# Kernel tuning notes

Hardware: AMD Instinct MI355X
Metric: run time of the kernel (lower is better)

Reference implementation:

```python
import jax, jax.numpy as jnp
import numpy as np

N = 50000
E = 800000
IN_CH = 128
HID = 32
HEADS = 8
OUT_CH = 64
NEG_SLOPE = 0.2  # PyG GATConv default


def setup_inputs() -> dict:
    key = jax.random.key(0)
    ks = jax.random.split(key, 12)
    x = jax.random.normal(ks[0], (N, IN_CH), dtype=jnp.float32)
    edge_index = jax.random.randint(ks[1], (2, E), 0, N, dtype=jnp.int64)
    s = 0.1
    return {
        "x": x,
        "edge_index": edge_index,
        "W1": jax.random.normal(ks[2], (IN_CH, HEADS * HID), dtype=jnp.float32) * s,
        "att_src1": jax.random.normal(ks[3], (HEADS, HID), dtype=jnp.float32) * s,
        "att_dst1": jax.random.normal(ks[4], (HEADS, HID), dtype=jnp.float32) * s,
        "b1": jnp.zeros((HEADS * HID,), dtype=jnp.float32),
        "W2": jax.random.normal(ks[5], (HEADS * HID, OUT_CH), dtype=jnp.float32) * s,
        "att_src2": jax.random.normal(ks[6], (1, OUT_CH), dtype=jnp.float32) * s,
        "att_dst2": jax.random.normal(ks[7], (1, OUT_CH), dtype=jnp.float32) * s,
        "b2": jnp.zeros((OUT_CH,), dtype=jnp.float32),
    }


def _gat_layer(x, src, dst, n, W, a_src, a_dst, b, concat):
    # x: [N, F_in]; src/dst: [E']; W: [F_in, H*C]; a_*: [H, C]
    H, C = a_src.shape
    h = (x @ W).reshape(-1, H, C)                       # [N, H, C]
    alpha_s = jnp.einsum('nhc,hc->nh', h, a_src)        # [N, H]
    alpha_d = jnp.einsum('nhc,hc->nh', h, a_dst)        # [N, H]
    alpha = alpha_s[src] + alpha_d[dst]                 # [E', H]
    alpha = jax.nn.leaky_relu(alpha, NEG_SLOPE)
    # segment (per-destination-node) softmax over incoming edges
    m = jax.ops.segment_max(alpha, dst, num_segments=n)     # [n, H]
    e = jnp.exp(alpha - m[dst])
    denom = jax.ops.segment_sum(e, dst, num_segments=n)     # [n, H]
    coef = e / denom[dst]                                   # [E', H]
    msg = h[src] * coef[:, :, None]                         # [E', H, C]
    out = jax.ops.segment_sum(msg, dst, num_segments=n)     # [n, H, C]
    out = out.reshape(n, H * C) if concat else out.mean(axis=1)
    return out + b


def reference(x, edge_index, W1, att_src1, att_dst1, b1, W2, att_src2, att_dst2, b2):
    n = x.shape[0]
    # PyG GATConv default: add self-loops
    loop = jnp.arange(n, dtype=edge_index.dtype)
    src = jnp.concatenate([edge_index[0], loop])
    dst = jnp.concatenate([edge_index[1], loop])
    # eval mode: F.dropout and attention dropout are identity
    h = _gat_layer(x, src, dst, n, W1, att_src1, att_dst1, b1, concat=True)
    h = jax.nn.elu(h)
    out = _gat_layer(h, src, dst, n, W2, att_src2, att_dst2, b2, concat=False)
    return out
```

## Files before the change

### kernel.cpp

```cpp
#include <hip/hip_runtime.h>
#include <hip/hip_bf16.h>
#include <math.h>

#define N_NODES 50000
#define N_EDGES 800000
#define E_TOT   (N_EDGES + N_NODES)
#define IN_CH 128
#define HID 32
#define HEADS 8
#define OUT_CH 64
#define NEG_SLOPE 0.2f
#define NBLK 196
#define G1BLK 3125
#define G2BLK 782
#define ABLK 12500
#define LOG2E 1.4426950408889634f

typedef __attribute__((ext_vector_type(8))) short bf16x8;
typedef __attribute__((ext_vector_type(4))) float f32x4;

__device__ __forceinline__ float lrelu(float x) { return x > 0.f ? x : NEG_SLOPE * x; }
__device__ __forceinline__ float explrelu(float z) {
    return exp2f(fmaxf(z * LOG2E, z * (NEG_SLOPE * LOG2E)));
}

__device__ __forceinline__ unsigned short f2bf(float f) {
    unsigned int u = __float_as_uint(f);
    unsigned int r = (u + 0x7FFFu + ((u >> 16) & 1u)) >> 16;
    return (unsigned short)r;
}
__device__ __forceinline__ float bf2f(unsigned short u) {
    return __uint_as_float(((unsigned int)u) << 16);
}
__device__ __forceinline__ float bflo(unsigned int u) {
    return __uint_as_float(u << 16);
}
__device__ __forceinline__ float bfhi(unsigned int u) {
    return __uint_as_float(u & 0xFFFF0000u);
}

__global__ void rank_kernel(const int* __restrict__ ei, int* __restrict__ deg,
                            int* __restrict__ rank) {
    int e = blockIdx.x * blockDim.x + threadIdx.x;
    if (e >= E_TOT) return;
    int d = (e < N_EDGES) ? ei[N_EDGES + e] : (e - N_EDGES);
    rank[e] = atomicAdd(&deg[d], 1);
}

__global__ void scan1_kernel(const int* __restrict__ deg, int* __restrict__ off,
                             int* __restrict__ bsum) {
    __shared__ int s[256];
    int b = blockIdx.x, t = threadIdx.x, g = b * 256 + t;
    int v = (g < N_NODES) ? deg[g] : 0;
    s[t] = v;
    __syncthreads();
    for (int d = 1; d < 256; d <<= 1) {
        int o = (t >= d) ? s[t - d] : 0;
        __syncthreads();
        s[t] += o;
        __syncthreads();
    }
    if (g < N_NODES) off[g] = s[t] - v;
    if (t == 255) bsum[b] = s[t];
}

__global__ void scan2_kernel(int* __restrict__ bsum, int nb) {
    __shared__ int s[256];
    int t = threadIdx.x;
    int v = (t < nb) ? bsum[t] : 0;
    s[t] = v;
    __syncthreads();
    for (int d = 1; d < 256; d <<= 1) {
        int o = (t >= d) ? s[t - d] : 0;
        __syncthreads();
        s[t] += o;
        __syncthreads();
    }
    if (t < nb) bsum[t] = s[t] - v;
}

__global__ void scan3_kernel(int* __restrict__ off, const int* __restrict__ bsum) {
    int b = blockIdx.x, t = threadIdx.x, g = b * 256 + t;
    if (g < N_NODES) off[g] += bsum[b];
    if (g == 0) off[N_NODES] = E_TOT;
}

__global__ void place_kernel(const int* __restrict__ ei, const int* __restrict__ off,
                             const int* __restrict__ rank, int* __restrict__ ssrc) {
    int e = blockIdx.x * blockDim.x + threadIdx.x;
    if (e >= E_TOT) return;
    int s, d;
    if (e < N_EDGES) { s = ei[e]; d = ei[N_EDGES + e]; }
    else             { s = d = e - N_EDGES; }
    ssrc[off[d] + rank[e]] = s;
}

__global__ void w1cast_kernel(const float* __restrict__ W1,
                              unsigned short* __restrict__ W1t) {
    int i = blockIdx.x * 256 + threadIdx.x;
    int col = i >> 7, k = i & 127;
    W1t[i] = f2bf(W1[k * 256 + col]);
}

__global__ void w2cast_kernel(const float* __restrict__ W2,
                              unsigned short* __restrict__ W2t) {
    int i = blockIdx.x * 256 + threadIdx.x;
    int col = i >> 8, k = i & 255;
    W2t[i] = f2bf(W2[k * 64 + col]);
}

__global__ __launch_bounds__(256) void gemm1_mfma(
    const float* __restrict__ x, const unsigned short* __restrict__ W1t,
    const float* __restrict__ att_s, const float* __restrict__ att_d,
    unsigned short* __restrict__ h1b, float* __restrict__ as1, float* __restrict__ ad1) {
    int t = threadIdx.x;
    int lane = t & 63;
    int w = t >> 6;
    int lrow = lane & 15;
    int kg = lane >> 4;
    int row0 = blockIdx.x * 16;
    int gr = row0 + lrow;
    f32x4 acc0 = {0.f, 0.f, 0.f, 0.f};
    f32x4 acc1 = {0.f, 0.f, 0.f, 0.f};
    f32x4 acc2 = {0.f, 0.f, 0.f, 0.f};
    f32x4 acc3 = {0.f, 0.f, 0.f, 0.f};
#pragma unroll
    for (int ks = 0; ks < 4; ++ks) {
        const float* ap = &x[(size_t)gr * IN_CH + ks * 32 + kg * 8];
        float4 a0 = *(const float4*)ap;
        float4 a1 = *(const float4*)(ap + 4);
        union { bf16x8 v; unsigned int u[4]; } A;
        A.u[0] = ((unsigned)f2bf(a0.y) << 16) | f2bf(a0.x);
        A.u[1] = ((unsigned)f2bf(a0.w) << 16) | f2bf(a0.z);
        A.u[2] = ((unsigned)f2bf(a1.y) << 16) | f2bf(a1.x);
        A.u[3] = ((unsigned)f2bf(a1.w) << 16) | f2bf(a1.z);
        union { bf16x8 v; uint4 u; } B0, B1, B2, B3;
        int kb = ks * 32 + kg * 8;
        B0.u = *(const uint4*)&W1t[(size_t)(w * 64 + 0 * 16 + lrow) * IN_CH + kb];
        B1.u = *(const uint4*)&W1t[(size_t)(w * 64 + 1 * 16 + lrow) * IN_CH + kb];
        B2.u = *(const uint4*)&W1t[(size_t)(w * 64 + 2 * 16 + lrow) * IN_CH + kb];
        B3.u = *(const uint4*)&W1t[(size_t)(w * 64 + 3 * 16 + lrow) * IN_CH + kb];
        acc0 = __builtin_amdgcn_mfma_f32_16x16x32_bf16(A.v, B0.v, acc0, 0, 0, 0);
        acc1 = __builtin_amdgcn_mfma_f32_16x16x32_bf16(A.v, B1.v, acc1, 0, 0, 0);
        acc2 = __builtin_amdgcn_mfma_f32_16x16x32_bf16(A.v, B2.v, acc2, 0, 0, 0);
        acc3 = __builtin_amdgcn_mfma_f32_16x16x32_bf16(A.v, B3.v, acc3, 0, 0, 0);
    }
    float s0 = att_s[w * 64 + 0 * 16 + lrow], d0 = att_d[w * 64 + 0 * 16 + lrow];
    float s1 = att_s[w * 64 + 1 * 16 + lrow], d1 = att_d[w * 64 + 1 * 16 + lrow];
    float s2 = att_s[w * 64 + 2 * 16 + lrow], d2 = att_d[w * 64 + 2 * 16 + lrow];
    float s3 = att_s[w * 64 + 3 * 16 + lrow], d3 = att_d[w * 64 + 3 * 16 + lrow];
#pragma unroll
    for (int r = 0; r < 4; ++r) {
        int orow = row0 + kg * 4 + r;
        h1b[(size_t)orow * 256 + w * 64 +  0 + lrow] = f2bf(acc0[r]);
        h1b[(size_t)orow * 256 + w * 64 + 16 + lrow] = f2bf(acc1[r]);
        h1b[(size_t)orow * 256 + w * 64 + 32 + lrow] = f2bf(acc2[r]);
        h1b[(size_t)orow * 256 + w * 64 + 48 + lrow] = f2bf(acc3[r]);
        float p0 = acc0[r] * s0 + acc1[r] * s1;
        float q0 = acc0[r] * d0 + acc1[r] * d1;
        float p1 = acc2[r] * s2 + acc3[r] * s3;
        float q1 = acc2[r] * d2 + acc3[r] * d3;
        p0 += __shfl_xor(p0, 1); q0 += __shfl_xor(q0, 1);
        p1 += __shfl_xor(p1, 1); q1 += __shfl_xor(q1, 1);
        p0 += __shfl_xor(p0, 2); q0 += __shfl_xor(q0, 2);
        p1 += __shfl_xor(p1, 2); q1 += __shfl_xor(q1, 2);
        p0 += __shfl_xor(p0, 4); q0 += __shfl_xor(q0, 4);
        p1 += __shfl_xor(p1, 4); q1 += __shfl_xor(q1, 4);
        p0 += __shfl_xor(p0, 8); q0 += __shfl_xor(q0, 8);
        p1 += __shfl_xor(p1, 8); q1 += __shfl_xor(q1, 8);
        if (lrow == 0) {
            as1[orow * HEADS + 2 * w]     = p0;
            ad1[orow * HEADS + 2 * w]     = q0;
            as1[orow * HEADS + 2 * w + 1] = p1;
            ad1[orow * HEADS + 2 * w + 1] = q1;
        }
    }
}

__global__ __launch_bounds__(256) void agg1_kernel(
    const int* __restrict__ off, const int* __restrict__ ssrc,
    const unsigned short* __restrict__ h1b, const float* __restrict__ as1,
    const float* __restrict__ ad1, const float* __restrict__ b1,
    unsigned short* __restrict__ houtb) {
    int t = threadIdx.x;
    int lane = t & 63;
    int n = blockIdx.x * 4 + (t >> 6);
    int h    = lane >> 3;
    int e8   = lane & 7;
    int c    = lane & 31;
    int hh   = c >> 2;
    int half = lane >> 5;
    int start = off[n], end = off[n + 1];
    int last = end - 1;
    float ad_w = ad1[n * HEADS + e8];
    float acc[8];
#pragma unroll
    for (int j = 0; j < 8; ++j) acc[j] = 0.f;
    float den = 0.f;
    int sv = ssrc[min(start + e8, last)];
    int se = __shfl(sv, h);
    float av = as1[se * HEADS + e8];
    const unsigned short* base = h1b + c * 8;
    uint4 g0 = *(const uint4*)&base[(unsigned)__shfl(sv, 0 + half) * 256];
    uint4 g1 = *(const uint4*)&base[(unsigned)__shfl(sv, 2 + half) * 256];
    uint4 g2 = *(const uint4*)&base[(unsigned)__shfl(sv, 4 + half) * 256];
    uint4 g3 = *(const uint4*)&base[(unsigned)__shfl(sv, 6 + half) * 256];
    for (int i = start; i < end; i += 8) {
        int inext = i + 8;
        int sv_n = ssrc[min(inext + e8, last)];
        int se_n = __shfl(sv_n, h);
        float av_n = as1[se_n * HEADS + e8];
        uint4 n0 = *(const uint4*)&base[(unsigned)__shfl(sv_n, 0 + half) * 256];
        uint4 n1 = *(const uint4*)&base[(unsigned)__shfl(sv_n, 2 + half) * 256];
        uint4 n2 = *(const uint4*)&base[(unsigned)__shfl(sv_n, 4 + half) * 256];
        uint4 n3 = *(const uint4*)&base[(unsigned)__shfl(sv_n, 6 + half) * 256];
        float wv = explrelu(av + ad_w);
        float w0 = __shfl(wv, (0 + half) * 8 + hh);
        float w1 = __shfl(wv, (2 + half) * 8 + hh);
        float w2 = __shfl(wv, (4 + half) * 8 + hh);
        float w3 = __shfl(wv, (6 + half) * 8 + hh);
        w0 = (i + 0 + half < end) ? w0 : 0.f;
        w1 = (i + 2 + half < end) ? w1 : 0.f;
        w2 = (i + 4 + half < end) ? w2 : 0.f;
        w3 = (i + 6 + half < end) ? w3 : 0.f;
        den += w0 + w1 + w2 + w3;
        acc[0] = fmaf(w0, bflo(g0.x), acc[0]); acc[1] = fmaf(w0, bfhi(g0.x), acc[1]);
        acc[2] = fmaf(w0, bflo(g0.y), acc[2]); acc[3] = fmaf(w0, bfhi(g0.y), acc[3]);
        acc[4] = fmaf(w0, bflo(g0.z), acc[4]); acc[5] = fmaf(w0, bfhi(g0.z), acc[5]);
        acc[6] = fmaf(w0, bflo(g0.w), acc[6]); acc[7] = fmaf(w0, bfhi(g0.w), acc[7]);
        acc[0] = fmaf(w1, bflo(g1.x), acc[0]); acc[1] = fmaf(w1, bfhi(g1.x), acc[1]);
        acc[2] = fmaf(w1, bflo(g1.y), acc[2]); acc[3] = fmaf(w1, bfhi(g1.y), acc[3]);
        acc[4] = fmaf(w1, bflo(g1.z), acc[4]); acc[5] = fmaf(w1, bfhi(g1.z), acc[5]);
        acc[6] = fmaf(w1, bflo(g1.w), acc[6]); acc[7] = fmaf(w1, bfhi(g1.w), acc[7]);
        acc[0] = fmaf(w2, bflo(g2.x), acc[0]); acc[1] = fmaf(w2, bfhi(g2.x), acc[1]);
        acc[2] = fmaf(w2, bflo(g2.y), acc[2]); acc[3] = fmaf(w2, bfhi(g2.y), acc[3]);
        acc[4] = fmaf(w2, bflo(g2.z), acc[4]); acc[5] = fmaf(w2, bfhi(g2.z), acc[5]);
        acc[6] = fmaf(w2, bflo(g2.w), acc[6]); acc[7] = fmaf(w2, bfhi(g2.w), acc[7]);
        acc[0] = fmaf(w3, bflo(g3.x), acc[0]); acc[1] = fmaf(w3, bfhi(g3.x), acc[1]);
        acc[2] = fmaf(w3, bflo(g3.y), acc[2]); acc[3] = fmaf(w3, bfhi(g3.y), acc[3]);
        acc[4] = fmaf(w3, bflo(g3.z), acc[4]); acc[5] = fmaf(w3, bfhi(g3.z), acc[5]);
        acc[6] = fmaf(w3, bflo(g3.w), acc[6]); acc[7] = fmaf(w3, bfhi(g3.w), acc[7]);
        g0 = n0; g1 = n1; g2 = n2; g3 = n3;
        sv = sv_n; av = av_n;
    }
#pragma unroll
    for (int j = 0; j < 8; ++j) acc[j] += __shfl_xor(acc[j], 32);
    den += __shfl_xor(den, 32);
    if (lane < 32) {
        float r = __builtin_amdgcn_rcpf(den);
        float4 b0 = *(const float4*)&b1[c * 8];
        float4 b4 = *(const float4*)&b1[c * 8 + 4];
        float v0 = fmaf(acc[0], r, b0.x);
        float v1 = fmaf(acc[1], r, b0.y);
        float v2 = fmaf(acc[2], r, b0.z);
        float v3 = fmaf(acc[3], r, b0.w);
        float v4 = fmaf(acc[4], r, b4.x);
        float v5 = fmaf(acc[5], r, b4.y);
        float v6 = fmaf(acc[6], r, b4.z);
        float v7 = fmaf(acc[7], r, b4.w);
        v0 = v0 > 0.f ? v0 : expm1f(v0);
        v1 = v1 > 0.f ? v1 : expm1f(v1);
        v2 = v2 > 0.f ? v2 : expm1f(v2);
        v3 = v3 > 0.f ? v3 : expm1f(v3);
        v4 = v4 > 0.f ? v4 : expm1f(v4);
        v5 = v5 > 0.f ? v5 : expm1f(v5);
        v6 = v6 > 0.f ? v6 : expm1f(v6);
        v7 = v7 > 0.f ? v7 : expm1f(v7);
        uint4 ob;
        ob.x = (unsigned)f2bf(v0) | ((unsigned)f2bf(v1) << 16);
        ob.y = (unsigned)f2bf(v2) | ((unsigned)f2bf(v3) << 16);
        ob.z = (unsigned)f2bf(v4) | ((unsigned)f2bf(v5) << 16);
        ob.w = (unsigned)f2bf(v6) | ((unsigned)f2bf(v7) << 16);
        *(uint4*)&houtb[(unsigned)n * 256 + c * 8] = ob;
    }
}

__global__ __launch_bounds__(256) void gemm2_mfma(
    const unsigned short* __restrict__ hinb, const unsigned short* __restrict__ W2t,
    const float* __restrict__ att_s2, const float* __restrict__ att_d2,
    unsigned short* __restrict__ h2b, float* __restrict__ as2, float* __restrict__ ad2) {
    int t = threadIdx.x;
    int lane = t & 63;
    int w = t >> 6;
    int lrow = lane & 15;
    int kg = lane >> 4;
    int row0 = blockIdx.x * 64 + w * 16;
    int gr = min(row0 + lrow, N_NODES - 1);
    f32x4 acc0 = {0.f, 0.f, 0.f, 0.f};
    f32x4 acc1 = {0.f, 0.f, 0.f, 0.f};
    f32x4 acc2 = {0.f, 0.f, 0.f, 0.f};
    f32x4 acc3 = {0.f, 0.f, 0.f, 0.f};
#pragma unroll
    for (int ks = 0; ks < 8; ++ks) {
        int kb = ks * 32 + kg * 8;
        union { bf16x8 v; uint4 u; } A, B0, B1, B2, B3;
        A.u  = *(const uint4*)&hinb[(size_t)gr * 256 + kb];
        B0.u = *(const uint4*)&W2t[(size_t)(0 * 16 + lrow) * 256 + kb];
        B1.u = *(const uint4*)&W2t[(size_t)(1 * 16 + lrow) * 256 + kb];
        B2.u = *(const uint4*)&W2t[(size_t)(2 * 16 + lrow) * 256 + kb];
        B3.u = *(const uint4*)&W2t[(size_t)(3 * 16 + lrow) * 256 + kb];
        acc0 = __builtin_amdgcn_mfma_f32_16x16x32_bf16(A.v, B0.v, acc0, 0, 0, 0);
        acc1 = __builtin_amdgcn_mfma_f32_16x16x32_bf16(A.v, B1.v, acc1, 0, 0, 0);
        acc2 = __builtin_amdgcn_mfma_f32_16x16x32_bf16(A.v, B2.v, acc2, 0, 0, 0);
        acc3 = __builtin_amdgcn_mfma_f32_16x16x32_bf16(A.v, B3.v, acc3, 0, 0, 0);
    }
    float s0 = att_s2[ 0 + lrow], d0 = att_d2[ 0 + lrow];
    float s1 = att_s2[16 + lrow], d1 = att_d2[16 + lrow];
    float s2 = att_s2[32 + lrow], d2 = att_d2[32 + lrow];
    float s3 = att_s2[48 + lrow], d3 = att_d2[48 + lrow];
#pragma unroll
    for (int r = 0; r < 4; ++r) {
        int orow = row0 + kg * 4 + r;
        float p = acc0[r] * s0 + acc1[r] * s1 + acc2[r] * s2 + acc3[r] * s3;
        float q = acc0[r] * d0 + acc1[r] * d1 + acc2[r] * d2 + acc3[r] * d3;
        p += __shfl_xor(p, 1); q += __shfl_xor(q, 1);
        p += __shfl_xor(p, 2); q += __shfl_xor(q, 2);
        p += __shfl_xor(p, 4); q += __shfl_xor(q, 4);
        p += __shfl_xor(p, 8); q += __shfl_xor(q, 8);
        if (orow < N_NODES) {
            h2b[(size_t)orow * 64 +  0 + lrow] = f2bf(acc0[r]);
            h2b[(size_t)orow * 64 + 16 + lrow] = f2bf(acc1[r]);
            h2b[(size_t)orow * 64 + 32 + lrow] = f2bf(acc2[r]);
            h2b[(size_t)orow * 64 + 48 + lrow] = f2bf(acc3[r]);
            if (lrow == 0) { as2[orow] = p; ad2[orow] = q; }
        }
    }
}

__global__ __launch_bounds__(256) void agg2_kernel(
    const int* __restrict__ off, const int* __restrict__ ssrc,
    const unsigned short* __restrict__ h2b, const float* __restrict__ as2,
    const float* __restrict__ ad2, const float* __restrict__ b2,
    float* __restrict__ out) {
    int t = threadIdx.x;
    int lane = t & 63;
    int e8 = lane & 7;
    int q = lane & 15;
    int quarter = lane >> 4;
    int n = blockIdx.x * 4 + (t >> 6);
    int start = off[n], end = off[n + 1];
    int last = end - 1;
    float adv = ad2[n];
    float acc[4];
#pragma unroll
    for (int j = 0; j < 4; ++j) acc[j] = 0.f;
    float den = 0.f;
    int sv = ssrc[min(start + e8, last)];
    float av = as2[sv];
    for (int i = start; i < end; i += 8) {
        int inext = i + 8;
        int sv_n = ssrc[min(inext + e8, last)];
        float av_n = as2[sv_n];
        float wv = explrelu(av + adv);
#pragma unroll
        for (int k = 0; k < 2; ++k) {
            int me = 4 * k + quarter;
            float wj = __shfl(wv, me);
            int   sj = __shfl(sv, me);
            wj = (i + me < end) ? wj : 0.f;
            uint2 u = *(const uint2*)&h2b[(unsigned)sj * 64 + q * 4];
            den += wj;
            acc[0] = fmaf(wj, bflo(u.x), acc[0]);
            acc[1] = fmaf(wj, bfhi(u.x), acc[1]);
            acc[2] = fmaf(wj, bflo(u.y), acc[2]);
            acc[3] = fmaf(wj, bfhi(u.y), acc[3]);
        }
        sv = sv_n; av = av_n;
    }
#pragma unroll
    for (int j = 0; j < 4; ++j) {
        acc[j] += __shfl_xor(acc[j], 16);
        acc[j] += __shfl_xor(acc[j], 32);
    }
    den += __shfl_xor(den, 16);
    den += __shfl_xor(den, 32);
    if (lane < 16) {
        float r = __builtin_amdgcn_rcpf(den);
        float4 bv = *(const float4*)&b2[q * 4];
        float4 o;
        o.x = fmaf(acc[0], r, bv.x);
        o.y = fmaf(acc[1], r, bv.y);
        o.z = fmaf(acc[2], r, bv.z);
        o.w = fmaf(acc[3], r, bv.w);
        *(float4*)&out[(unsigned)n * 64 + q * 4] = o;
    }
}

extern "C" void kernel_launch(void* const* d_in, const int* in_sizes, int n_in,
                              void* d_out, int out_size, void* d_ws, size_t ws_size,
                              hipStream_t stream) {
    const float* x    = (const float*)d_in[0];
    const int*   ei   = (const int*)d_in[1];
    const float* W1   = (const float*)d_in[2];
    const float* ats1 = (const float*)d_in[3];
    const float* atd1 = (const float*)d_in[4];
    const float* b1   = (const float*)d_in[5];
    const float* W2   = (const float*)d_in[6];
    const float* ats2 = (const float*)d_in[7];
    const float* atd2 = (const float*)d_in[8];
    const float* b2   = (const float*)d_in[9];
    float* out = (float*)d_out;

    char* ws = (char*)d_ws;
    size_t o = 0;
    auto alloc = [&](size_t bytes) { size_t r = o; o = (o + bytes + 255) & ~255UL; return r; };
    unsigned short* h1b   = (unsigned short*)(ws + alloc((size_t)N_NODES * 256 * 2));
    unsigned short* h2inb = (unsigned short*)(ws + alloc((size_t)N_NODES * 256 * 2));
    unsigned short* h2b   = (unsigned short*)(ws + alloc((size_t)N_NODES * 64 * 2));
    unsigned short* W1t   = (unsigned short*)(ws + alloc((size_t)256 * 128 * 2));
    unsigned short* W2t   = (unsigned short*)(ws + alloc((size_t)64 * 256 * 2));
    float* as1  = (float*)(ws + alloc((size_t)N_NODES * HEADS * 4));
    float* ad1  = (float*)(ws + alloc((size_t)N_NODES * HEADS * 4));
    float* as2  = (float*)(ws + alloc((size_t)N_NODES * 4));
    float* ad2  = (float*)(ws + alloc((size_t)N_NODES * 4));
    int*   deg  = (int*)(ws + alloc((size_t)N_NODES * 4));
    int*   off  = (int*)(ws + alloc((size_t)(N_NODES + 1) * 4));
    int*   bsum = (int*)(ws + alloc(256 * 4));
    int*   rank = (int*)(ws + alloc((size_t)E_TOT * 4));
    int*   ssrc = (int*)(ws + alloc((size_t)E_TOT * 4));

    (void)hipMemsetAsync(deg, 0, (size_t)N_NODES * 4, stream);
    int eblk = (E_TOT + 255) / 256;
    rank_kernel<<<eblk, 256, 0, stream>>>(ei, deg, rank);
    scan1_kernel<<<NBLK, 256, 0, stream>>>(deg, off, bsum);
    scan2_kernel<<<1, 256, 0, stream>>>(bsum, NBLK);
    scan3_kernel<<<NBLK, 256, 0, stream>>>(off, bsum);
    place_kernel<<<eblk, 256, 0, stream>>>(ei, off, rank, ssrc);

    w1cast_kernel<<<128, 256, 0, stream>>>(W1, W1t);
    gemm1_mfma<<<G1BLK, 256, 0, stream>>>(x, W1t, ats1, atd1, h1b, as1, ad1);
    agg1_kernel<<<ABLK, 256, 0, stream>>>(off, ssrc, h1b, as1, ad1, b1, h2inb);

    w2cast_kernel<<<64, 256, 0, stream>>>(W2, W2t);
    gemm2_mfma<<<G2BLK, 256, 0, stream>>>(h2inb, W2t, ats2, atd2, h2b, as2, ad2);
    agg2_kernel<<<ABLK, 256, 0, stream>>>(off, ssrc, h2b, as2, ad2, b2, out);
}
```

Baseline: 225.1 us.

## Fuse rank counting, GEMM1 and W2 cast into one launch; pad degree counters

Merges the edge-rank atomic kernel, the first MFMA GEMM and the W2 bf16 cast into a single grid whose block index picks the role. Independent work can then overlap and two launches go away. Degree counters are padded to one per 64 bytes to reduce atomic contention on shared cache lines. In exchange the degree array is sixteen times larger, so the memset and the scan read more memory.

```diff
diff --git a/kernel.cpp b/kernel.cpp
--- a/kernel.cpp
+++ b/kernel.cpp
@@ -11,6 +11,7 @@
 #define OUT_CH 64
 #define NEG_SLOPE 0.2f
 #define NBLK 196
+#define RBLK 3321
 #define G1BLK 3125
 #define G2BLK 782
 #define ABLK 12500
@@ -37,62 +38,6 @@
 }
 __device__ __forceinline__ float bfhi(unsigned int u) {
     return __uint_as_float(u & 0xFFFF0000u);
-}
-
-__global__ void rank_kernel(const int* __restrict__ ei, int* __restrict__ deg,
-                            int* __restrict__ rank) {
-    int e = blockIdx.x * blockDim.x + threadIdx.x;
-    if (e >= E_TOT) return;
-    int d = (e < N_EDGES) ? ei[N_EDGES + e] : (e - N_EDGES);
-    rank[e] = atomicAdd(&deg[d], 1);
-}
-
-__global__ void scan1_kernel(const int* __restrict__ deg, int* __restrict__ off,
-                             int* __restrict__ bsum) {
-    __shared__ int s[256];
-    int b = blockIdx.x, t = threadIdx.x, g = b * 256 + t;
-    int v = (g < N_NODES) ? deg[g] : 0;
-    s[t] = v;
-    __syncthreads();
-    for (int d = 1; d < 256; d <<= 1) {
-        int o = (t >= d) ? s[t - d] : 0;
-        __syncthreads();
-        s[t] += o;
-        __syncthreads();
-    }
-    if (g < N_NODES) off[g] = s[t] - v;
-    if (t == 255) bsum[b] = s[t];
-}
-
-__global__ void scan2_kernel(int* __restrict__ bsum, int nb) {
-    __shared__ int s[256];
-    int t = threadIdx.x;
-    int v = (t < nb) ? bsum[t] : 0;
-    s[t] = v;
-    __syncthreads();
-    for (int d = 1; d < 256; d <<= 1) {
-        int o = (t >= d) ? s[t - d] : 0;
-        __syncthreads();
-        s[t] += o;
-        __syncthreads();
-    }
-    if (t < nb) bsum[t] = s[t] - v;
-}
-
-__global__ void scan3_kernel(int* __restrict__ off, const int* __restrict__ bsum) {
-    int b = blockIdx.x, t = threadIdx.x, g = b * 256 + t;
-    if (g < N_NODES) off[g] += bsum[b];
-    if (g == 0) off[N_NODES] = E_TOT;
-}
-
-__global__ void place_kernel(const int* __restrict__ ei, const int* __restrict__ off,
-                             const int* __restrict__ rank, int* __restrict__ ssrc) {
-    int e = blockIdx.x * blockDim.x + threadIdx.x;
-    if (e >= E_TOT) return;
-    int s, d;
-    if (e < N_EDGES) { s = ei[e]; d = ei[N_EDGES + e]; }
-    else             { s = d = e - N_EDGES; }
-    ssrc[off[d] + rank[e]] = s;
 }
 
 __global__ void w1cast_kernel(const float* __restrict__ W1,
@@ -102,23 +47,16 @@
     W1t[i] = f2bf(W1[k * 256 + col]);
 }
 
-__global__ void w2cast_kernel(const float* __restrict__ W2,
-                              unsigned short* __restrict__ W2t) {
-    int i = blockIdx.x * 256 + threadIdx.x;
-    int col = i >> 8, k = i & 255;
-    W2t[i] = f2bf(W2[k * 64 + col]);
-}
-
-__global__ __launch_bounds__(256) void gemm1_mfma(
+__device__ __forceinline__ void gemm1_body(
+    int blk, int t,
     const float* __restrict__ x, const unsigned short* __restrict__ W1t,
     const float* __restrict__ att_s, const float* __restrict__ att_d,
     unsigned short* __restrict__ h1b, float* __restrict__ as1, float* __restrict__ ad1) {
-    int t = threadIdx.x;
     int lane = t & 63;
     int w = t >> 6;
     int lrow = lane & 15;
     int kg = lane >> 4;
-    int row0 = blockIdx.x * 16;
+    int row0 = blk * 16;
     int gr = row0 + lrow;
     f32x4 acc0 = {0.f, 0.f, 0.f, 0.f};
     f32x4 acc1 = {0.f, 0.f, 0.f, 0.f};
@@ -175,6 +113,76 @@
             ad1[orow * HEADS + 2 * w + 1] = q1;
         }
     }
+}
+
+__global__ __launch_bounds__(256) void fused1_kernel(
+    const int* __restrict__ ei, int* __restrict__ deg2, int* __restrict__ rank,
+    const float* __restrict__ x, const unsigned short* __restrict__ W1t,
+    const float* __restrict__ att_s, const float* __restrict__ att_d,
+    unsigned short* __restrict__ h1b, float* __restrict__ as1, float* __restrict__ ad1,
+    const float* __restrict__ W2, unsigned short* __restrict__ W2t) {
+    int b = blockIdx.x;
+    if (b < RBLK) {
+        int e = b * 256 + threadIdx.x;
+        if (e < E_TOT) {
+            int d = (e < N_EDGES) ? ei[N_EDGES + e] : (e - N_EDGES);
+            rank[e] = atomicAdd(&deg2[d * 16], 1);
+        }
+    } else if (b < RBLK + G1BLK) {
+        gemm1_body(b - RBLK, threadIdx.x, x, W1t, att_s, att_d, h1b, as1, ad1);
+    } else {
+        int i = (b - RBLK - G1BLK) * 256 + threadIdx.x;
+        int col = i >> 8, k = i & 255;
+        W2t[i] = f2bf(W2[k * 64 + col]);
+    }
+}
+
+__global__ void scan1_kernel(const int* __restrict__ deg2, int* __restrict__ off,
+                             int* __restrict__ bsum) {
+    __shared__ int s[256];
+    int b = blockIdx.x, t = threadIdx.x, g = b * 256 + t;
+    int v = (g < N_NODES) ? deg2[g * 16] : 0;
+    s[t] = v;
+    __syncthreads();
+    for (int d = 1; d < 256; d <<= 1) {
+        int o = (t >= d) ? s[t - d] : 0;
+        __syncthreads();
+        s[t] += o;
+        __syncthreads();
+    }
+    if (g < N_NODES) off[g] = s[t] - v;
+    if (t == 255) bsum[b] = s[t];
+}
+
+__global__ void scan2_kernel(int* __restrict__ bsum, int nb) {
+    __shared__ int s[256];
+    int t = threadIdx.x;
+    int v = (t < nb) ? bsum[t] : 0;
+    s[t] = v;
+    __syncthreads();
+    for (int d = 1; d < 256; d <<= 1) {
+        int o = (t >= d) ? s[t - d] : 0;
+        __syncthreads();
+        s[t] += o;
+        __syncthreads();
+    }
+    if (t < nb) bsum[t] = s[t] - v;
+}
+
+__global__ void scan3_kernel(int* __restrict__ off, const int* __restrict__ bsum) {
+    int b = blockIdx.x, t = threadIdx.x, g = b * 256 + t;
+    if (g < N_NODES) off[g] += bsum[b];
+    if (g == 0) off[N_NODES] = E_TOT;
+}
+
+__global__ void place_kernel(const int* __restrict__ ei, const int* __restrict__ off,
+                             const int* __restrict__ rank, int* __restrict__ ssrc) {
+    int e = blockIdx.x * blockDim.x + threadIdx.x;
+    if (e >= E_TOT) return;
+    int s, d;
+    if (e < N_EDGES) { s = ei[e]; d = ei[N_EDGES + e]; }
+    else             { s = d = e - N_EDGES; }
+    ssrc[off[d] + rank[e]] = s;
 }
 
 __global__ __launch_bounds__(256) void agg1_kernel(
@@ -413,25 +421,25 @@
     float* ad1  = (float*)(ws + alloc((size_t)N_NODES * HEADS * 4));
     float* as2  = (float*)(ws + alloc((size_t)N_NODES * 4));
     float* ad2  = (float*)(ws + alloc((size_t)N_NODES * 4));
-    int*   deg  = (int*)(ws + alloc((size_t)N_NODES * 4));
+    int*   deg2 = (int*)(ws + alloc((size_t)N_NODES * 16 * 4));
     int*   off  = (int*)(ws + alloc((size_t)(N_NODES + 1) * 4));
     int*   bsum = (int*)(ws + alloc(256 * 4));
     int*   rank = (int*)(ws + alloc((size_t)E_TOT * 4));
     int*   ssrc = (int*)(ws + alloc((size_t)E_TOT * 4));
 
-    (void)hipMemsetAsync(deg, 0, (size_t)N_NODES * 4, stream);
+    (void)hipMemsetAsync(deg2, 0, (size_t)N_NODES * 16 * 4, stream);
     int eblk = (E_TOT + 255) / 256;
-    rank_kernel<<<eblk, 256, 0, stream>>>(ei, deg, rank);
-    scan1_kernel<<<NBLK, 256, 0, stream>>>(deg, off, bsum);
+
+    w1cast_kernel<<<128, 256, 0, stream>>>(W1, W1t);
+    fused1_kernel<<<RBLK + G1BLK + 64, 256, 0, stream>>>(
+        ei, deg2, rank, x, W1t, ats1, atd1, h1b, as1, ad1, W2, W2t);
+    scan1_kernel<<<NBLK, 256, 0, stream>>>(deg2, off, bsum);
     scan2_kernel<<<1, 256, 0, stream>>>(bsum, NBLK);
     scan3_kernel<<<NBLK, 256, 0, stream>>>(off, bsum);
     place_kernel<<<eblk, 256, 0, stream>>>(ei, off, rank, ssrc);
 
-    w1cast_kernel<<<128, 256, 0, stream>>>(W1, W1t);
-    gemm1_mfma<<<G1BLK, 256, 0, stream>>>(x, W1t, ats1, atd1, h1b, as1, ad1);
     agg1_kernel<<<ABLK, 256, 0, stream>>>(off, ssrc, h1b, as1, ad1, b1, h2inb);
 
-    w2cast_kernel<<<64, 256, 0, stream>>>(W2, W2t);
     gemm2_mfma<<<G2BLK, 256, 0, stream>>>(h2inb, W2t, ats2, atd2, h2b, as2, ad2);
     agg2_kernel<<<ABLK, 256, 0, stream>>>(off, ssrc, h2b, as2, ad2, b2, out);
 }
```

New measurement: 219.0 us. 1.03x faster.

## Replace global-atomic CSR build with two-level bucketed counting sort

Applied to the files above, without the earlier changes.

Builds the destination-sorted edge list with a two-pass radix-style sort: per-chunk shared-memory histograms over 128-node buckets, a scan of the bucket-by-chunk counts, a scatter into bucket order, then a per-bucket shared-memory sort into per-node order. This replaces the per-edge global atomicAdd on node degrees and the random scatter, aiming to cut global atomic contention and scattered writes. It adds temporary src/dst arrays and an extra pass, and only 159 blocks for hist/scatter may underuse the GPU.

```diff
diff --git a/kernel.cpp b/kernel.cpp
--- a/kernel.cpp
+++ b/kernel.cpp
@@ -10,16 +10,20 @@
 #define HEADS 8
 #define OUT_CH 64
 #define NEG_SLOPE 0.2f
-#define NBLK 196
 #define G1BLK 3125
 #define G2BLK 782
 #define ABLK 12500
 #define LOG2E 1.4426950408889634f
 
+#define CHUNK_E 5376
+#define NCHUNK 159
+#define NBUCK 391
+#define CNT_TOT (NBUCK * NCHUNK)
+#define SBLK 243
+
 typedef __attribute__((ext_vector_type(8))) short bf16x8;
 typedef __attribute__((ext_vector_type(4))) float f32x4;
 
-__device__ __forceinline__ float lrelu(float x) { return x > 0.f ? x : NEG_SLOPE * x; }
 __device__ __forceinline__ float explrelu(float z) {
     return exp2f(fmaxf(z * LOG2E, z * (NEG_SLOPE * LOG2E)));
 }
@@ -39,19 +43,29 @@
     return __uint_as_float(u & 0xFFFF0000u);
 }
 
-__global__ void rank_kernel(const int* __restrict__ ei, int* __restrict__ deg,
-                            int* __restrict__ rank) {
-    int e = blockIdx.x * blockDim.x + threadIdx.x;
-    if (e >= E_TOT) return;
-    int d = (e < N_EDGES) ? ei[N_EDGES + e] : (e - N_EDGES);
-    rank[e] = atomicAdd(&deg[d], 1);
-}
-
-__global__ void scan1_kernel(const int* __restrict__ deg, int* __restrict__ off,
-                             int* __restrict__ bsum) {
+__global__ __launch_bounds__(256) void hist1_kernel(const int* __restrict__ ei,
+                                                    int* __restrict__ cnt) {
+    __shared__ int hist[NBUCK];
+    int t = threadIdx.x, blk = blockIdx.x;
+    for (int j = t; j < NBUCK; j += 256) hist[j] = 0;
+    __syncthreads();
+#pragma unroll
+    for (int i = 0; i < 21; ++i) {
+        int e = blk * CHUNK_E + i * 256 + t;
+        if (e < E_TOT) {
+            int d = (e < N_EDGES) ? ei[N_EDGES + e] : (e - N_EDGES);
+            atomicAdd(&hist[d >> 7], 1);
+        }
+    }
+    __syncthreads();
+    for (int j = t; j < NBUCK; j += 256) cnt[j * NCHUNK + blk] = hist[j];
+}
+
+__global__ void sscan1_kernel(const int* __restrict__ cnt, int* __restrict__ pos,
+                              int* __restrict__ bsum) {
     __shared__ int s[256];
     int b = blockIdx.x, t = threadIdx.x, g = b * 256 + t;
-    int v = (g < N_NODES) ? deg[g] : 0;
+    int v = (g < CNT_TOT) ? cnt[g] : 0;
     s[t] = v;
     __syncthreads();
     for (int d = 1; d < 256; d <<= 1) {
@@ -60,11 +74,11 @@
         s[t] += o;
         __syncthreads();
     }
-    if (g < N_NODES) off[g] = s[t] - v;
+    if (g < CNT_TOT) pos[g] = s[t] - v;
     if (t == 255) bsum[b] = s[t];
 }
 
-__global__ void scan2_kernel(int* __restrict__ bsum, int nb) {
+__global__ void sscan2_kernel(int* __restrict__ bsum, int nb) {
     __shared__ int s[256];
     int t = threadIdx.x;
     int v = (t < nb) ? bsum[t] : 0;
@@ -79,20 +93,68 @@
     if (t < nb) bsum[t] = s[t] - v;
 }
 
-__global__ void scan3_kernel(int* __restrict__ off, const int* __restrict__ bsum) {
+__global__ void sscan3_kernel(int* __restrict__ pos, const int* __restrict__ bsum) {
     int b = blockIdx.x, t = threadIdx.x, g = b * 256 + t;
-    if (g < N_NODES) off[g] += bsum[b];
-    if (g == 0) off[N_NODES] = E_TOT;
-}
-
-__global__ void place_kernel(const int* __restrict__ ei, const int* __restrict__ off,
-                             const int* __restrict__ rank, int* __restrict__ ssrc) {
-    int e = blockIdx.x * blockDim.x + threadIdx.x;
-    if (e >= E_TOT) return;
-    int s, d;
-    if (e < N_EDGES) { s = ei[e]; d = ei[N_EDGES + e]; }
-    else             { s = d = e - N_EDGES; }
-    ssrc[off[d] + rank[e]] = s;
+    if (g < CNT_TOT) pos[g] += bsum[b];
+}
+
+__global__ __launch_bounds__(256) void scat1_kernel(const int* __restrict__ ei,
+                                                    const int* __restrict__ pos,
+                                                    int* __restrict__ tmp_s,
+                                                    int* __restrict__ tmp_d) {
+    __shared__ int cur[NBUCK];
+    int t = threadIdx.x, blk = blockIdx.x;
+    for (int j = t; j < NBUCK; j += 256) cur[j] = pos[j * NCHUNK + blk];
+    __syncthreads();
+#pragma unroll
+    for (int i = 0; i < 21; ++i) {
+        int e = blk * CHUNK_E + i * 256 + t;
+        if (e < E_TOT) {
+            int s, d;
+            if (e < N_EDGES) { s = ei[e]; d = ei[N_EDGES + e]; }
+            else             { s = d = e - N_EDGES; }
+            int p = atomicAdd(&cur[d >> 7], 1);
+            tmp_s[p] = s;
+            tmp_d[p] = d;
+        }
+    }
+}
+
+__global__ __launch_bounds__(256) void l2group_kernel(
+    const int* __restrict__ pos, const int* __restrict__ tmp_s,
+    const int* __restrict__ tmp_d, int* __restrict__ off, int* __restrict__ ssrc) {
+    __shared__ int nc[128];
+    __shared__ int sc[128];
+    int b = blockIdx.x, t = threadIdx.x;
+    int seg_start = pos[b * NCHUNK];
+    int seg_end = (b + 1 < NBUCK) ? pos[(b + 1) * NCHUNK] : E_TOT;
+    if (t < 128) nc[t] = 0;
+    __syncthreads();
+    for (int i = seg_start + t; i < seg_end; i += 256)
+        atomicAdd(&nc[tmp_d[i] & 127], 1);
+    __syncthreads();
+    if (t < 128) sc[t] = nc[t];
+    __syncthreads();
+    for (int dd = 1; dd < 128; dd <<= 1) {
+        int v = 0;
+        if (t < 128 && t >= dd) v = sc[t - dd];
+        __syncthreads();
+        if (t < 128) sc[t] += v;
+        __syncthreads();
+    }
+    if (t < 128) {
+        int excl = sc[t] - nc[t];
+        int node = b * 128 + t;
+        if (node < N_NODES) off[node] = seg_start + excl;
+        nc[t] = seg_start + excl;
+    }
+    if (b == 0 && t == 0) off[N_NODES] = E_TOT;
+    __syncthreads();
+    for (int i = seg_start + t; i < seg_end; i += 256) {
+        int d = tmp_d[i];
+        int p = atomicAdd(&nc[d & 127], 1);
+        ssrc[p] = tmp_s[i];
+    }
 }
 
 __global__ void w1cast_kernel(const float* __restrict__ W1,
@@ -413,19 +475,20 @@
     float* ad1  = (float*)(ws + alloc((size_t)N_NODES * HEADS * 4));
     float* as2  = (float*)(ws + alloc((size_t)N_NODES * 4));
     float* ad2  = (float*)(ws + alloc((size_t)N_NODES * 4));
-    int*   deg  = (int*)(ws + alloc((size_t)N_NODES * 4));
+    int*   cnt  = (int*)(ws + alloc((size_t)CNT_TOT * 4));
+    int*   pos  = (int*)(ws + alloc((size_t)CNT_TOT * 4));
+    int*   bsum = (int*)(ws + alloc(256 * 4));
     int*   off  = (int*)(ws + alloc((size_t)(N_NODES + 1) * 4));
-    int*   bsum = (int*)(ws + alloc(256 * 4));
-    int*   rank = (int*)(ws + alloc((size_t)E_TOT * 4));
-    int*   ssrc = (int*)(ws + alloc((size_t)E_TOT * 4));
-
-    (void)hipMemsetAsync(deg, 0, (size_t)N_NODES * 4, stream);
-    int eblk = (E_TOT + 255) / 256;
-    rank_kernel<<<eblk, 256, 0, stream>>>(ei, deg, rank);
-    scan1_kernel<<<NBLK, 256, 0, stream>>>(deg, off, bsum);
-    scan2_kernel<<<1, 256, 0, stream>>>(bsum, NBLK);
-    scan3_kernel<<<NBLK, 256, 0, stream>>>(off, bsum);
-    place_kernel<<<eblk, 256, 0, stream>>>(ei, off, rank, ssrc);
+    int*   tmp_s = (int*)(ws + alloc((size_t)E_TOT * 4));
+    int*   tmp_d = (int*)(ws + alloc((size_t)E_TOT * 4));
+    int*   ssrc  = (int*)(ws + alloc((size_t)E_TOT * 4));
+
+    hist1_kernel<<<NCHUNK, 256, 0, stream>>>(ei, cnt);
+    sscan1_kernel<<<SBLK, 256, 0, stream>>>(cnt, pos, bsum);
+    sscan2_kernel<<<1, 256, 0, stream>>>(bsum, SBLK);
+    sscan3_kernel<<<SBLK, 256, 0, stream>>>(pos, bsum);
+    scat1_kernel<<<NCHUNK, 256, 0, stream>>>(ei, pos, tmp_s, tmp_d);
+    l2group_kernel<<<NBUCK, 256, 0, stream>>>(pos, tmp_s, tmp_d, off, ssrc);
 
     w1cast_kernel<<<128, 256, 0, stream>>>(W1, W1t);
     gemm1_mfma<<<G1BLK, 256, 0, stream>>>(x, W1t, ats1, atd1, h1b, as1, ad1);
```

Measured after the change: 206.1 us. 1.09x faster.
